# Optimization experiments

Measured on AMD Instinct MI355X. Metric: run time of the kernel, lower is better.

## Reference

```python
import jax, jax.numpy as jnp
import numpy as np

MARGIN = 0.1  # hinge margin (kcal/mol), matches init kwarg
B = 8192
N_GROUPS = 16
MAX_GALLOYL = 12


def setup_inputs() -> dict:
    key = jax.random.key(0)
    k1, k2, k3 = jax.random.split(key, 3)
    pred = jax.random.normal(k1, (B,), dtype=jnp.float32)
    galloyl_units = jax.random.randint(k2, (B,), 0, MAX_GALLOYL, dtype=jnp.int64)
    group = jax.random.randint(k3, (B,), 0, N_GROUPS, dtype=jnp.int64)
    return {"pred": pred, "galloyl_units": galloyl_units, "group": group}


def reference(pred, galloyl_units, group):
    # Ordered pairs (i, j) with galloyl[i] > galloyl[j] correspond one-to-one
    # to the unordered pairs the original double loop visits (hi -> lo).
    pred = pred.reshape(-1)
    galloyl_units = galloyl_units.reshape(-1)
    same_group = group[:, None] == group[None, :]            # [B, B]
    higher = galloyl_units[:, None] > galloyl_units[None, :]  # [B, B]
    mask = same_group & higher
    # violation = relu(pred_hi - pred_lo + margin)^2
    diff = pred[:, None] - pred[None, :] + jnp.float32(MARGIN)
    viol = jnp.where(mask, jnp.square(jax.nn.relu(diff)), jnp.float32(0.0))
    count = jnp.sum(mask)
    total = jnp.sum(viol)
    # reduction='mean' over violating-eligible pairs; 0.0 if no pairs
    loss = jnp.where(count > 0, total / jnp.maximum(count, 1).astype(pred.dtype), jnp.float32(0.0))
    return loss
```

## Files before the change

kernel.cpp:

```cpp
#include <hip/hip_runtime.h>


constexpr int       NG     = 16;
constexpr int       NSUB   = 4;
constexpr int       NBLK   = NG * NSUB;
constexpr int       NT     = 1024;
constexpr int       CAP    = 1024;
constexpr float     MARGIN = 0.1f;
constexpr long long MAGIC  = 0x3FC0FFEE5EED5EEDll;

__global__ __launch_bounds__(NT)
void mono_one_kernel(const float* __restrict__ pred,
                     const int*   __restrict__ gall,
                     const int*   __restrict__ grp,
                     int n,
                     double*    __restrict__ part_sum,
                     long long* __restrict__ part_cnt,
                     long long* __restrict__ flags,
                     float*     __restrict__ out)
{
    __shared__ int2   s_pg[CAP];
    __shared__ int    s_cnt;
    __shared__ double s_ws[NT / 64];
    __shared__ int    s_wc[NT / 64];

    const int tid  = threadIdx.x;
    const int bid  = blockIdx.x;
    const int g    = bid & (NG - 1);
    const int sub  = bid >> 4;
    const int lane = tid & 63;

    if (tid == 0) s_cnt = 0;
    __syncthreads();

    for (int base = tid * 4; base < n; base += NT * 4) {
        const int4   gv = *reinterpret_cast<const int4*>(grp  + base);
        const float4 pv = *reinterpret_cast<const float4*>(pred + base);
        const int4   av = *reinterpret_cast<const int4*>(gall + base);

        #define COMPACT(GC, PC, AC)                                              \
        {                                                                        \
            const bool c = (GC == g);                                            \
            const unsigned long long m = __ballot(c);                            \
            int b0 = 0;                                                          \
            if (lane == 0 && m) b0 = atomicAdd(&s_cnt, __popcll(m));             \
            b0 = __shfl(b0, 0);                                                  \
            if (c) {                                                             \
                const int s = b0 + __popcll(m & ((1ull << lane) - 1ull));        \
                if (s < CAP) s_pg[s] = make_int2(__float_as_int(PC), AC);        \
            }                                                                    \
        }
        COMPACT(gv.x, pv.x, av.x)
        COMPACT(gv.y, pv.y, av.y)
        COMPACT(gv.z, pv.z, av.z)
        COMPACT(gv.w, pv.w, av.w)
        #undef COMPACT
    }
    __syncthreads();

    const int size = min(s_cnt, CAP);
    const int jbeg = (sub * size) >> 2;
    const int jend = ((sub + 1) * size) >> 2;

    float pim = 0.0f;
    int   gi  = -1;
    if (tid < size) {
        const int2 v = s_pg[tid];
        pim = __int_as_float(v.x) + MARGIN;
        gi  = v.y;
    }

    float vsum = 0.0f;
    int   vcnt = 0;
    if ((int)(tid & ~63u) < size) {
        #pragma unroll 4
        for (int t = jbeg; t < jend; ++t) {
            const int2  v = s_pg[t];
            const bool  m = gi > v.y;
            const float d = pim - __int_as_float(v.x);
            float       r = fmaxf(d, 0.0f);
            r = m ? r : 0.0f;
            vsum = fmaf(r, r, vsum);
            vcnt += (int)m;
        }
    }

    double w = (double)vsum;
    int    c = vcnt;
    for (int off = 32; off > 0; off >>= 1) {
        w += __shfl_down(w, off);
        c += __shfl_down(c, off);
    }
    if ((tid & 63) == 0) { s_ws[tid >> 6] = w; s_wc[tid >> 6] = c; }
    __syncthreads();
    if (tid == 0) {
        double    bs = 0.0;
        long long bc = 0;
        #pragma unroll
        for (int wv = 0; wv < NT / 64; ++wv) { bs += s_ws[wv]; bc += (long long)s_wc[wv]; }
        __hip_atomic_store(&part_sum[bid], bs, __ATOMIC_RELAXED, __HIP_MEMORY_SCOPE_AGENT);
        __hip_atomic_store(&part_cnt[bid], bc, __ATOMIC_RELAXED, __HIP_MEMORY_SCOPE_AGENT);
        __hip_atomic_store(&flags[bid], MAGIC, __ATOMIC_RELEASE, __HIP_MEMORY_SCOPE_AGENT);
    }

    if (bid == 0 && tid < NBLK) {
        while (__hip_atomic_load(&flags[tid], __ATOMIC_ACQUIRE,
                                 __HIP_MEMORY_SCOPE_AGENT) != MAGIC)
            __builtin_amdgcn_s_sleep(1);

        double    ts = __hip_atomic_load(&part_sum[tid], __ATOMIC_RELAXED,
                                         __HIP_MEMORY_SCOPE_AGENT);
        long long tc = __hip_atomic_load(&part_cnt[tid], __ATOMIC_RELAXED,
                                         __HIP_MEMORY_SCOPE_AGENT);
        for (int off = 32; off > 0; off >>= 1) {
            ts += __shfl_down(ts, off);
            tc += __shfl_down(tc, off);
        }
        if (tid == 0)
            out[0] = (tc > 0) ? (float)(ts / (double)tc) : 0.0f;
    }
}

extern "C" void kernel_launch(void* const* d_in, const int* in_sizes, int n_in,
                              void* d_out, int out_size, void* d_ws, size_t ws_size,
                              hipStream_t stream)
{
    const float* pred = (const float*)d_in[0];
    const int*   gall = (const int*)d_in[1];
    const int*   grp  = (const int*)d_in[2];
    const int    n    = in_sizes[0];

    char* ws = (char*)d_ws;
    double*    part_sum = (double*)ws;
    long long* part_cnt = (long long*)(ws + NBLK * sizeof(double));
    long long* flags    = (long long*)(ws + 2 * NBLK * sizeof(double));

    mono_one_kernel<<<NBLK, NT, 0, stream>>>(pred, gall, grp, n,
                                             part_sum, part_cnt, flags,
                                             (float*)d_out);
}
```

Before: 14.76 us.

## Split pair work across 256 blocks via index-range j-compaction

Raises the per-group split from 4 to 16 blocks, for 256 blocks in total, so more CUs are busy. Each block now compacts its j-partners only from its own index slice of the input, into a second small shared buffer with CAPJ=128. Ballots are batched so there is one LDS atomic per four elements, and there is a fast path for n == 8192. The final reduction loops over multiple flags per lane. The cost is more blocks re-scanning the full input and a fixed j-capacity that could overflow on other input distributions.

```diff
diff --git a/kernel.cpp b/kernel.cpp
--- a/kernel.cpp
+++ b/kernel.cpp
@@ -2,10 +2,11 @@
 
 
 constexpr int       NG     = 16;
-constexpr int       NSUB   = 4;
+constexpr int       NSUB   = 16;
 constexpr int       NBLK   = NG * NSUB;
 constexpr int       NT     = 1024;
 constexpr int       CAP    = 1024;
+constexpr int       CAPJ   = 128;
 constexpr float     MARGIN = 0.1f;
 constexpr long long MAGIC  = 0x3FC0FFEE5EED5EEDll;
 
@@ -19,8 +20,9 @@
                      long long* __restrict__ flags,
                      float*     __restrict__ out)
 {
-    __shared__ int2   s_pg[CAP];
-    __shared__ int    s_cnt;
+    __shared__ int2   s_i[CAP];
+    __shared__ int2   s_j[CAPJ];
+    __shared__ int    s_cnt, s_jcnt;
     __shared__ double s_ws[NT / 64];
     __shared__ int    s_wc[NT / 64];
 
@@ -30,42 +32,85 @@
     const int sub  = bid >> 4;
     const int lane = tid & 63;
 
-    if (tid == 0) s_cnt = 0;
+    const int jlo = (int)(((long long)sub * n) / NSUB);
+    const int jw  = (int)(((long long)(sub + 1) * n) / NSUB) - jlo;
+
+    if (tid == 0) { s_cnt = 0; s_jcnt = 0; }
     __syncthreads();
 
-    for (int base = tid * 4; base < n; base += NT * 4) {
-        const int4   gv = *reinterpret_cast<const int4*>(grp  + base);
-        const float4 pv = *reinterpret_cast<const float4*>(pred + base);
-        const int4   av = *reinterpret_cast<const int4*>(gall + base);
+    auto compact4 = [&](int4 gv, float4 pv, int4 av, int base) {
+        const bool c0 = gv.x == g, c1 = gv.y == g, c2 = gv.z == g, c3 = gv.w == g;
+        const unsigned long long m0 = __ballot(c0), m1 = __ballot(c1),
+                                 m2 = __ballot(c2), m3 = __ballot(c3);
+        const int p0 = __popcll(m0), p1 = __popcll(m1), p2 = __popcll(m2);
+        int b = 0;
+        if (lane == 0) {
+            const int t = p0 + p1 + p2 + __popcll(m3);
+            if (t) b = atomicAdd(&s_cnt, t);
+        }
+        b = __shfl(b, 0);
+        const unsigned long long below = (1ull << lane) - 1ull;
+        if (c0) { const int s = b + __popcll(m0 & below);               if (s < CAP) s_i[s] = make_int2(__float_as_int(pv.x), av.x); }
+        if (c1) { const int s = b + p0 + __popcll(m1 & below);          if (s < CAP) s_i[s] = make_int2(__float_as_int(pv.y), av.y); }
+        if (c2) { const int s = b + p0 + p1 + __popcll(m2 & below);     if (s < CAP) s_i[s] = make_int2(__float_as_int(pv.z), av.z); }
+        if (c3) { const int s = b + p0 + p1 + p2 + __popcll(m3 & below);if (s < CAP) s_i[s] = make_int2(__float_as_int(pv.w), av.w); }
 
-        #define COMPACT(GC, PC, AC)                                              \
-        {                                                                        \
-            const bool c = (GC == g);                                            \
-            const unsigned long long m = __ballot(c);                            \
-            int b0 = 0;                                                          \
-            if (lane == 0 && m) b0 = atomicAdd(&s_cnt, __popcll(m));             \
-            b0 = __shfl(b0, 0);                                                  \
-            if (c) {                                                             \
-                const int s = b0 + __popcll(m & ((1ull << lane) - 1ull));        \
-                if (s < CAP) s_pg[s] = make_int2(__float_as_int(PC), AC);        \
-            }                                                                    \
+        const bool j0 = c0 && (unsigned)(base + 0 - jlo) < (unsigned)jw;
+        const bool j1 = c1 && (unsigned)(base + 1 - jlo) < (unsigned)jw;
+        const bool j2 = c2 && (unsigned)(base + 2 - jlo) < (unsigned)jw;
+        const bool j3 = c3 && (unsigned)(base + 3 - jlo) < (unsigned)jw;
+        const unsigned long long q0 = __ballot(j0), q1 = __ballot(j1),
+                                 q2 = __ballot(j2), q3 = __ballot(j3);
+        if (q0 | q1 | q2 | q3) {
+            const int r0 = __popcll(q0), r1 = __popcll(q1), r2 = __popcll(q2);
+            int bj = 0;
+            if (lane == 0) bj = atomicAdd(&s_jcnt, r0 + r1 + r2 + __popcll(q3));
+            bj = __shfl(bj, 0);
+            if (j0) { const int s = bj + __popcll(q0 & below);               if (s < CAPJ) s_j[s] = make_int2(__float_as_int(pv.x), av.x); }
+            if (j1) { const int s = bj + r0 + __popcll(q1 & below);          if (s < CAPJ) s_j[s] = make_int2(__float_as_int(pv.y), av.y); }
+            if (j2) { const int s = bj + r0 + r1 + __popcll(q2 & below);     if (s < CAPJ) s_j[s] = make_int2(__float_as_int(pv.z), av.z); }
+            if (j3) { const int s = bj + r0 + r1 + r2 + __popcll(q3 & below);if (s < CAPJ) s_j[s] = make_int2(__float_as_int(pv.w), av.w); }
         }
-        COMPACT(gv.x, pv.x, av.x)
-        COMPACT(gv.y, pv.y, av.y)
-        COMPACT(gv.z, pv.z, av.z)
-        COMPACT(gv.w, pv.w, av.w)
-        #undef COMPACT
+    };
+
+    if (n == NT * 8) {
+        const int b0 = tid * 4, b1 = b0 + NT * 4;
+        const int4   gv0 = *reinterpret_cast<const int4*>(grp  + b0);
+        const int4   gv1 = *reinterpret_cast<const int4*>(grp  + b1);
+        const float4 pv0 = *reinterpret_cast<const float4*>(pred + b0);
+        const float4 pv1 = *reinterpret_cast<const float4*>(pred + b1);
+        const int4   av0 = *reinterpret_cast<const int4*>(gall + b0);
+        const int4   av1 = *reinterpret_cast<const int4*>(gall + b1);
+        compact4(gv0, pv0, av0, b0);
+        compact4(gv1, pv1, av1, b1);
+    } else {
+        for (int base = tid * 4; base + 3 < n; base += NT * 4) {
+            const int4   gv = *reinterpret_cast<const int4*>(grp  + base);
+            const float4 pv = *reinterpret_cast<const float4*>(pred + base);
+            const int4   av = *reinterpret_cast<const int4*>(gall + base);
+            compact4(gv, pv, av, base);
+        }
+        for (int idx = (n & ~3) + tid; idx < n; idx += NT) {
+            if (grp[idx] == g) {
+                const int2 v = make_int2(__float_as_int(pred[idx]), gall[idx]);
+                const int s = atomicAdd(&s_cnt, 1);
+                if (s < CAP) s_i[s] = v;
+                if ((unsigned)(idx - jlo) < (unsigned)jw) {
+                    const int sj = atomicAdd(&s_jcnt, 1);
+                    if (sj < CAPJ) s_j[sj] = v;
+                }
+            }
+        }
     }
     __syncthreads();
 
     const int size = min(s_cnt, CAP);
-    const int jbeg = (sub * size) >> 2;
-    const int jend = ((sub + 1) * size) >> 2;
+    const int jn   = min(s_jcnt, CAPJ);
 
     float pim = 0.0f;
     int   gi  = -1;
     if (tid < size) {
-        const int2 v = s_pg[tid];
+        const int2 v = s_i[tid];
         pim = __int_as_float(v.x) + MARGIN;
         gi  = v.y;
     }
@@ -73,9 +118,8 @@
     float vsum = 0.0f;
     int   vcnt = 0;
     if ((int)(tid & ~63u) < size) {
-        #pragma unroll 4
-        for (int t = jbeg; t < jend; ++t) {
-            const int2  v = s_pg[t];
+        for (int t = 0; t < jn; ++t) {
+            const int2  v = s_j[t];
             const bool  m = gi > v.y;
             const float d = pim - __int_as_float(v.x);
             float       r = fmaxf(d, 0.0f);
@@ -103,15 +147,25 @@
         __hip_atomic_store(&flags[bid], MAGIC, __ATOMIC_RELEASE, __HIP_MEMORY_SCOPE_AGENT);
     }
 
-    if (bid == 0 && tid < NBLK) {
-        while (__hip_atomic_load(&flags[tid], __ATOMIC_ACQUIRE,
-                                 __HIP_MEMORY_SCOPE_AGENT) != MAGIC)
-            __builtin_amdgcn_s_sleep(1);
-
-        double    ts = __hip_atomic_load(&part_sum[tid], __ATOMIC_RELAXED,
-                                         __HIP_MEMORY_SCOPE_AGENT);
-        long long tc = __hip_atomic_load(&part_cnt[tid], __ATOMIC_RELAXED,
-                                         __HIP_MEMORY_SCOPE_AGENT);
+    if (bid == 0 && tid < 64) {
+        bool done = false;
+        while (!done) {
+            done = true;
+            #pragma unroll
+            for (int k = 0; k < NBLK / 64; ++k)
+                done &= (__hip_atomic_load(&flags[tid + 64 * k], __ATOMIC_ACQUIRE,
+                                           __HIP_MEMORY_SCOPE_AGENT) == MAGIC);
+            if (!done) __builtin_amdgcn_s_sleep(1);
+        }
+        double    ts = 0.0;
+        long long tc = 0;
+        #pragma unroll
+        for (int k = 0; k < NBLK / 64; ++k) {
+            ts += __hip_atomic_load(&part_sum[tid + 64 * k], __ATOMIC_RELAXED,
+                                    __HIP_MEMORY_SCOPE_AGENT);
+            tc += __hip_atomic_load(&part_cnt[tid + 64 * k], __ATOMIC_RELAXED,
+                                    __HIP_MEMORY_SCOPE_AGENT);
+        }
         for (int off = 32; off > 0; off >>= 1) {
             ts += __shfl_down(ts, off);
             tc += __shfl_down(tc, off);
```

New measurement: 13.86 us. 1.06x faster.
